# Performance work log

Measured on AMD Instinct MI355X. Metric: run time of the kernel, lower is better.

Reference implementation:

```python
import jax, jax.numpy as jnp
import numpy as np

GROUPS = 8
EPS = 1e-3  # keras GroupNormalization default epsilon


def group_norm(x, gamma, beta):
    # x: [B,H,W,C], groups over channel axis
    B, H, W, C = x.shape
    g = GROUPS
    xr = x.reshape(B, H, W, g, C // g)
    mean = jnp.mean(xr, axis=(1, 2, 4), keepdims=True)
    var = jnp.var(xr, axis=(1, 2, 4), keepdims=True)
    xn = (xr - mean) * jax.lax.rsqrt(var + EPS)
    xn = xn.reshape(B, H, W, C)
    return xn * gamma + beta


def setup_inputs() -> dict:
    key = jax.random.key(0)
    ks = jax.random.split(key, 6)
    B, H, W, C = 8, 64, 64, 64
    std = 0.02
    return {
        "x": jax.random.normal(ks[0], (B, H, W, C), dtype=jnp.float32),
        "gamma": jnp.ones((C,), dtype=jnp.float32),
        "beta": jnp.zeros((C,), dtype=jnp.float32),
        "wq": jax.random.normal(ks[1], (C, C), dtype=jnp.float32) * std,
        "bq": jnp.zeros((C,), dtype=jnp.float32),
        "wk": jax.random.normal(ks[2], (C, C), dtype=jnp.float32) * std,
        "bk": jnp.zeros((C,), dtype=jnp.float32),
        "wv": jax.random.normal(ks[3], (C, C), dtype=jnp.float32) * std,
        "bv": jnp.zeros((C,), dtype=jnp.float32),
        "wp": jax.random.normal(ks[4], (C, C), dtype=jnp.float32) * std,
        "bp": jnp.zeros((C,), dtype=jnp.float32),
    }


def reference(x, gamma, beta, wq, bq, wk, bk, wv, bv, wp, bp):
    B, H, W, C = x.shape
    scale = jnp.asarray(C, x.dtype) ** -0.5
    h = group_norm(x, gamma, beta)  # note: residual uses normalized input (as in source)
    q = h @ wq + bq
    k = h @ wk + bk
    v = h @ wv + bv
    # full O((HW)^2) score tensor, exactly as the original
    attn = jnp.einsum('bhwc,bHWc->bhwHW', q, k) * scale
    attn = jax.nn.softmax(attn.reshape(B, H, W, H * W), axis=-1)
    attn = attn.reshape(B, H, W, H, W)
    proj = jnp.einsum('bhwHW,bHWc->bhwc', attn, v)
    proj = proj @ wp + bp
    return h + proj
```

## Files before the change

kernel.cpp:

```cpp
#include <hip/hip_runtime.h>

#define NTOK 4096
#define CH 64
#define LOG2E 1.4426950408889634f

typedef __bf16 bf8 __attribute__((ext_vector_type(8)));
typedef __bf16 bf4 __attribute__((ext_vector_type(4)));
typedef _Float16 h8 __attribute__((ext_vector_type(8)));
typedef _Float16 h4 __attribute__((ext_vector_type(4)));
typedef __fp16 fp16x2 __attribute__((ext_vector_type(2)));
typedef float f4 __attribute__((ext_vector_type(4)));

__device__ __forceinline__ f4 mfma16(bf8 a, bf8 b, f4 c) {
    return __builtin_amdgcn_mfma_f32_16x16x32_bf16(a, b, c, 0, 0, 0);
}
__device__ __forceinline__ f4 mfma32h(h8 a, h8 b, f4 c) {
    return __builtin_amdgcn_mfma_f32_16x16x32_f16(a, b, c, 0, 0, 0);
}

__global__ __launch_bounds__(256) void pre_kernel(const float* __restrict__ wq,
                                                  const float* __restrict__ wk,
                                                  const float* __restrict__ wv,
                                                  const float* __restrict__ wp,
                                                  const float* __restrict__ x,
                                                  __bf16* __restrict__ wqt,
                                                  __bf16* __restrict__ wkt,
                                                  __bf16* __restrict__ wvt,
                                                  __bf16* __restrict__ wpt,
                                                  float* __restrict__ gpart) {
    int t = threadIdx.x;
    if (blockIdx.x < 4) {
        int m = blockIdx.x;
        const float* src = (m == 0) ? wq : (m == 1) ? wk : (m == 2) ? wv : wp;
        __bf16* dst      = (m == 0) ? wqt : (m == 1) ? wkt : (m == 2) ? wvt : wpt;
        __shared__ float s[64][65];
        for (int i = 0; i < 16; ++i) {
            int e = i * 256 + t;
            s[e >> 6][e & 63] = src[e];
        }
        __syncthreads();
        int o = t >> 2, seg = t & 3;
        for (int j = 0; j < 16; ++j) {
            int in = seg * 16 + j;
            dst[o * 64 + in] = (__bf16)s[in][o];
        }
        return;
    }
    int bid = blockIdx.x - 4;
    int b = bid >> 6, slab = bid & 63;
    const float4* xb = (const float4*)(x + (size_t)(b * NTOK + slab * 64) * CH);
    float s = 0.f, ss = 0.f;
    for (int i = 0; i < 4; ++i) {
        int row = (t >> 4) + i * 16;
        float4 v = xb[row * 16 + (t & 15)];
        s  += v.x + v.y + v.z + v.w;
        ss += v.x * v.x + v.y * v.y + v.z * v.z + v.w * v.w;
    }
    __shared__ float ls[256], lss[256];
    ls[t] = s; lss[t] = ss;
    __syncthreads();
    if (t < 8) {
        float a = 0.f, aa = 0.f;
        for (int p = 0; p < 16; ++p) {
            a  += ls[p * 16 + 2 * t]  + ls[p * 16 + 2 * t + 1];
            aa += lss[p * 16 + 2 * t] + lss[p * 16 + 2 * t + 1];
        }
        gpart[((b * 64 + slab) * 8 + t) * 2 + 0] = a;
        gpart[((b * 64 + slab) * 8 + t) * 2 + 1] = aa;
    }
}

__global__ __launch_bounds__(256) void qkv_gn(const float* __restrict__ x,
                                              const float* __restrict__ gpart,
                                              const float* __restrict__ gamma,
                                              const float* __restrict__ beta,
                                              const __bf16* __restrict__ wqt,
                                              const __bf16* __restrict__ wkt,
                                              const __bf16* __restrict__ wvt,
                                              const float* __restrict__ bq,
                                              const float* __restrict__ bk,
                                              const float* __restrict__ bv,
                                              __bf16* __restrict__ q,
                                              __bf16* __restrict__ k,
                                              _Float16* __restrict__ vT) {
    __shared__ __bf16 W[3][64][72];
    __shared__ __bf16 Hl[64][72];
    __shared__ _Float16 Vst[64][68];
    __shared__ float red[128];
    __shared__ float sstat[16];
    int t = threadIdx.x;
    size_t rowbase = (size_t)blockIdx.x * 64;
    int b = (int)(rowbase >> 12), tokbase = (int)(rowbase & 4095);
    if (t < 64) {
        int gi = t & 7, c = t >> 3;
        const float2* gp = (const float2*)gpart + (size_t)b * 512 + gi;
        float a = 0.f, aa = 0.f;
        for (int p = c * 8; p < c * 8 + 8; ++p) {
            float2 v = gp[(size_t)p * 8];
            a += v.x; aa += v.y;
        }
        red[t * 2] = a; red[t * 2 + 1] = aa;
    }
    for (int m = 0; m < 3; ++m) {
        const __bf16* src = (m == 0) ? wqt : (m == 1) ? wkt : wvt;
        for (int i = 0; i < 2; ++i) {
            int e = i * 256 + t, row = e >> 3, ch = e & 7;
            *(bf8*)&W[m][row][ch * 8] = *(const bf8*)(src + row * 64 + ch * 8);
        }
    }
    __syncthreads();
    if (t < 8) {
        float a = 0.f, aa = 0.f;
        for (int c = 0; c < 8; ++c) {
            a  += red[(c * 8 + t) * 2];
            aa += red[(c * 8 + t) * 2 + 1];
        }
        float mean = a * (1.f / 32768.f);
        float var = aa * (1.f / 32768.f) - mean * mean;
        sstat[t * 2 + 0] = mean;
        sstat[t * 2 + 1] = rsqrtf(var + 1e-3f);
    }
    __syncthreads();
    {
        int c4 = (t & 15) * 4, grp = c4 >> 3;
        float mean = sstat[grp * 2], rstd = sstat[grp * 2 + 1];
        float g0 = gamma[c4] * rstd, g1 = gamma[c4 + 1] * rstd,
              g2 = gamma[c4 + 2] * rstd, g3 = gamma[c4 + 3] * rstd;
        float b0 = beta[c4], b1 = beta[c4 + 1], b2 = beta[c4 + 2], b3 = beta[c4 + 3];
        const float4* xb = (const float4*)(x + rowbase * 64);
        for (int i = 0; i < 4; ++i) {
            int row = (t >> 4) + i * 16;
            float4 v = xb[row * 16 + (t & 15)];
            bf4 hv;
            hv[0] = (__bf16)((v.x - mean) * g0 + b0);
            hv[1] = (__bf16)((v.y - mean) * g1 + b1);
            hv[2] = (__bf16)((v.z - mean) * g2 + b2);
            hv[3] = (__bf16)((v.w - mean) * g3 + b3);
            *(bf4*)&Hl[row][c4] = hv;
        }
    }
    __syncthreads();
    int lane = t & 63, wave = t >> 6, quad = lane >> 4, l15 = lane & 15;
    bf8 a0 = *(const bf8*)&Hl[wave * 16 + l15][quad * 8];
    bf8 a1 = *(const bf8*)&Hl[wave * 16 + l15][32 + quad * 8];
    for (int m = 0; m < 3; ++m) {
        const float* bias = (m == 0) ? bq : (m == 1) ? bk : bv;
        float sc = (m == 0) ? 0.125f * LOG2E : 1.0f;
        for (int tt = 0; tt < 4; ++tt) {
            int col = l15 + 16 * tt;
            bf8 b0 = *(const bf8*)&W[m][col][quad * 8];
            bf8 b1 = *(const bf8*)&W[m][col][32 + quad * 8];
            f4 acc = {0.f, 0.f, 0.f, 0.f};
            acc = mfma16(a0, b0, acc);
            acc = mfma16(a1, b1, acc);
            float bb = bias[col];
            if (m == 2) {
                for (int r = 0; r < 4; ++r)
                    Vst[col][wave * 16 + quad * 4 + r] = (_Float16)(acc[r] + bb);
            } else {
                __bf16* dst = (m == 0) ? q : k;
                for (int r = 0; r < 4; ++r) {
                    float val = (acc[r] + bb) * sc;
                    dst[(rowbase + wave * 16 + quad * 4 + r) * 64 + col] = (__bf16)val;
                }
            }
        }
    }
    __syncthreads();
    {
        int d = wave * 16 + l15;
        for (int kb = 0; kb < 2; ++kb) {
            h4 lo = *(const h4*)&Vst[d][kb * 32 + quad * 4];
            h4 hi = *(const h4*)&Vst[d][kb * 32 + 16 + quad * 4];
            h8 o;
            o[0] = lo[0]; o[1] = lo[1]; o[2] = lo[2]; o[3] = lo[3];
            o[4] = hi[0]; o[5] = hi[1]; o[6] = hi[2]; o[7] = hi[3];
            _Float16* dst = vT + ((((size_t)b * 128 + (tokbase >> 5) + kb) * 4 + wave) * 64
                                  + lane) * 8;
            *(h8*)dst = o;
        }
    }
}

__device__ __forceinline__ void load_kv(const __bf16* kr0, const _Float16* vr, int quad,
                                        bf8 kf[4], h8 vf[4]) {
    kf[0] = *(const bf8*)(kr0 + quad * 8);
    kf[1] = *(const bf8*)(kr0 + 32 + quad * 8);
    kf[2] = *(const bf8*)(kr0 + 1024 + quad * 8);
    kf[3] = *(const bf8*)(kr0 + 1024 + 32 + quad * 8);
    vf[0] = *(const h8*)(vr);
    vf[1] = *(const h8*)(vr + 512);
    vf[2] = *(const h8*)(vr + 1024);
    vf[3] = *(const h8*)(vr + 1536);
}

__device__ __forceinline__ void compute32(const bf8 kf[4], const h8 vf[4],
                                          const bf8 aq[4][2], h8 ones,
                                          f4 acc[4][4], f4 acc_li[4]) {
#pragma unroll
    for (int s = 0; s < 4; ++s) {
        f4 St0 = {0.f, 0.f, 0.f, 0.f};
        f4 St1 = {0.f, 0.f, 0.f, 0.f};
        St0 = mfma16(kf[0], aq[s][0], St0);
        St0 = mfma16(kf[1], aq[s][1], St0);
        St1 = mfma16(kf[2], aq[s][0], St1);
        St1 = mfma16(kf[3], aq[s][1], St1);
        float p00 = __builtin_amdgcn_exp2f(St0[0]);
        float p01 = __builtin_amdgcn_exp2f(St0[1]);
        float p02 = __builtin_amdgcn_exp2f(St0[2]);
        float p03 = __builtin_amdgcn_exp2f(St0[3]);
        float p10 = __builtin_amdgcn_exp2f(St1[0]);
        float p11 = __builtin_amdgcn_exp2f(St1[1]);
        float p12 = __builtin_amdgcn_exp2f(St1[2]);
        float p13 = __builtin_amdgcn_exp2f(St1[3]);
        h8 pf;
        ((fp16x2*)&pf)[0] = __builtin_amdgcn_cvt_pkrtz(p00, p01);
        ((fp16x2*)&pf)[1] = __builtin_amdgcn_cvt_pkrtz(p02, p03);
        ((fp16x2*)&pf)[2] = __builtin_amdgcn_cvt_pkrtz(p10, p11);
        ((fp16x2*)&pf)[3] = __builtin_amdgcn_cvt_pkrtz(p12, p13);
        acc_li[s] = mfma32h(ones, pf, acc_li[s]);
        acc[s][0] = mfma32h(vf[0], pf, acc[s][0]);
        acc[s][1] = mfma32h(vf[1], pf, acc[s][1]);
        acc[s][2] = mfma32h(vf[2], pf, acc[s][2]);
        acc[s][3] = mfma32h(vf[3], pf, acc[s][3]);
    }
}

__global__ __launch_bounds__(256, 2) void attn_final(const __bf16* __restrict__ q,
                                                     const __bf16* __restrict__ k,
                                                     const _Float16* __restrict__ vt,
                                                     const __bf16* __restrict__ wpt,
                                                     const float* __restrict__ bp,
                                                     const float* __restrict__ x,
                                                     const float* __restrict__ gpart,
                                                     const float* __restrict__ gamma,
                                                     const float* __restrict__ beta,
                                                     float* __restrict__ out) {
    __shared__ _Float16 Om[2][64][72];
    __shared__ float sS[2][64];
    __shared__ __bf16 Wl[64][72];
    __shared__ __bf16 Ol[64][72];
    __shared__ float red[128];
    __shared__ float sstat[16], sg[64], sb[64];

    int bid = blockIdx.x;
    int qt = bid >> 3, b = bid & 7;
    int t = threadIdx.x, lane = t & 63, w = t >> 6, quad = lane >> 4, l15 = lane & 15;

    for (int i = 0; i < 2; ++i) {
        int e = i * 256 + t, row = e >> 3, ch = e & 7;
        *(bf8*)&Wl[row][ch * 8] = *(const bf8*)(wpt + row * 64 + ch * 8);
    }
    if (t < 64) { sg[t] = gamma[t]; sb[t] = beta[t]; }
    if (t < 64) {
        int gi = t & 7, c = t >> 3;
        const float2* gp = (const float2*)gpart + (size_t)b * 512 + gi;
        float a = 0.f, aa = 0.f;
        for (int p = c * 8; p < c * 8 + 8; ++p) {
            float2 v = gp[(size_t)p * 8];
            a += v.x; aa += v.y;
        }
        red[t * 2] = a; red[t * 2 + 1] = aa;
    }

    const __bf16* qbase = q + ((size_t)b * NTOK + qt * 64) * 64;
    bf8 aq[4][2];
    for (int s = 0; s < 4; ++s) {
        const __bf16* r = qbase + (s * 16 + l15) * 64;
        aq[s][0] = *(const bf8*)(r + quad * 8);
        aq[s][1] = *(const bf8*)(r + 32 + quad * 8);
    }
    const __bf16* kbase   = k  + ((size_t)b * NTOK + w * 1024) * 64;
    const _Float16* vbase = vt + (size_t)b * 262144 + (size_t)(w * 32) * 2048 + lane * 8;

    h8 ones;
#pragma unroll
    for (int j = 0; j < 8; ++j) ones[j] = (_Float16)1.f;

    f4 acc[4][4] = {};
    f4 acc_li[4] = {};

    bf8 kfA[4], kfB[4];
    h8 vfA[4], vfB[4];
    load_kv(kbase + (size_t)l15 * 64, vbase, quad, kfA, vfA);
    for (int it = 0; it < 32; it += 2) {
        load_kv(kbase + (size_t)((it + 1) * 32 + l15) * 64,
                vbase + (size_t)(it + 1) * 2048, quad, kfB, vfB);
        __builtin_amdgcn_s_setprio(1);
        compute32(kfA, vfA, aq, ones, acc, acc_li);
        __builtin_amdgcn_s_setprio(0);
        if (it + 2 < 32)
            load_kv(kbase + (size_t)((it + 2) * 32 + l15) * 64,
                    vbase + (size_t)(it + 2) * 2048, quad, kfA, vfA);
        __builtin_amdgcn_s_setprio(1);
        compute32(kfB, vfB, aq, ones, acc, acc_li);
        __builtin_amdgcn_s_setprio(0);
    }

    float li[4];
#pragma unroll
    for (int s = 0; s < 4; ++s) li[s] = acc_li[s][0];

    if (w >= 2) {
        for (int s = 0; s < 4; ++s) {
            for (int td = 0; td < 4; ++td) {
                h4 o4;
                for (int r = 0; r < 4; ++r) o4[r] = (_Float16)acc[s][td][r];
                *(h4*)&Om[w - 2][s * 16 + l15][td * 16 + quad * 4] = o4;
            }
            if (quad == 0) sS[w - 2][s * 16 + l15] = li[s];
        }
    }
    __syncthreads();
    if (t < 8) {
        float a = 0.f, aa = 0.f;
        for (int c = 0; c < 8; ++c) {
            a  += red[(c * 8 + t) * 2];
            aa += red[(c * 8 + t) * 2 + 1];
        }
        float mean = a * (1.f / 32768.f);
        float var = aa * (1.f / 32768.f) - mean * mean;
        sstat[t * 2 + 0] = mean;
        sstat[t * 2 + 1] = rsqrtf(var + 1e-3f);
    }
    if (w < 2) {
        for (int s = 0; s < 4; ++s) {
            for (int td = 0; td < 4; ++td) {
                h4 o4 = *(const h4*)&Om[w][s * 16 + l15][td * 16 + quad * 4];
                for (int r = 0; r < 4; ++r) acc[s][td][r] += (float)o4[r];
            }
            li[s] += sS[w][s * 16 + l15];
        }
    }
    __syncthreads();
    if (w < 2) {
        for (int s = 0; s < 4; ++s) {
            for (int td = 0; td < 4; ++td) {
                h4 o4;
                for (int r = 0; r < 4; ++r) o4[r] = (_Float16)acc[s][td][r];
                *(h4*)&Om[w][s * 16 + l15][td * 16 + quad * 4] = o4;
            }
            if (quad == 0) sS[w][s * 16 + l15] = li[s];
        }
    }
    __syncthreads();
    {
        int qq = t >> 2, ds = (t & 3) * 16;
        float inv = 1.f / (sS[0][qq] + sS[1][qq]);
        h8 a0 = *(const h8*)&Om[0][qq][ds];
        h8 b0 = *(const h8*)&Om[0][qq][ds + 8];
        h8 a1 = *(const h8*)&Om[1][qq][ds];
        h8 b1 = *(const h8*)&Om[1][qq][ds + 8];
        bf8 olo, ohi;
        for (int j = 0; j < 8; ++j) {
            olo[j] = (__bf16)(((float)a0[j] + (float)a1[j]) * inv);
            ohi[j] = (__bf16)(((float)b0[j] + (float)b1[j]) * inv);
        }
        *(bf8*)&Ol[qq][ds] = olo;
        *(bf8*)&Ol[qq][ds + 8] = ohi;
    }
    __syncthreads();
    size_t rowbase = ((size_t)b * NTOK + qt * 64) + w * 16;
    bf8 a0 = *(const bf8*)&Ol[w * 16 + l15][quad * 8];
    bf8 a1 = *(const bf8*)&Ol[w * 16 + l15][32 + quad * 8];
    for (int tt = 0; tt < 4; ++tt) {
        int col = l15 + 16 * tt;
        bf8 b0 = *(const bf8*)&Wl[col][quad * 8];
        bf8 b1 = *(const bf8*)&Wl[col][32 + quad * 8];
        f4 pacc = {0.f, 0.f, 0.f, 0.f};
        pacc = mfma16(a0, b0, pacc);
        pacc = mfma16(a1, b1, pacc);
        int grp = col >> 3;
        float mean = sstat[grp * 2], gs = sg[col] * sstat[grp * 2 + 1], bs = sb[col];
        float bias = bp[col];
        for (int r = 0; r < 4; ++r) {
            size_t gi = (rowbase + quad * 4 + r) * 64 + col;
            float h = (x[gi] - mean) * gs + bs;
            out[gi] = pacc[r] + bias + h;
        }
    }
}

extern "C" void kernel_launch(void* const* d_in, const int* in_sizes, int n_in,
                              void* d_out, int out_size, void* d_ws, size_t ws_size,
                              hipStream_t stream) {
    const float* x     = (const float*)d_in[0];
    const float* gamma = (const float*)d_in[1];
    const float* beta  = (const float*)d_in[2];
    const float* wq    = (const float*)d_in[3];
    const float* bq    = (const float*)d_in[4];
    const float* wk    = (const float*)d_in[5];
    const float* bk    = (const float*)d_in[6];
    const float* wv    = (const float*)d_in[7];
    const float* bv    = (const float*)d_in[8];
    const float* wp    = (const float*)d_in[9];
    const float* bp    = (const float*)d_in[10];
    float* out = (float*)d_out;

    char* ws = (char*)d_ws;
    const size_t MB = 1024 * 1024;
    __bf16*   qb   = (__bf16*)(ws);
    __bf16*   kb   = (__bf16*)(ws + 4 * MB);
    _Float16* vtb  = (_Float16*)(ws + 8 * MB);
    __bf16*   wqt  = (__bf16*)(ws + 12 * MB);
    __bf16*   wkt  = (__bf16*)(ws + 12 * MB + 8192);
    __bf16*   wvt  = (__bf16*)(ws + 12 * MB + 16384);
    __bf16*   wpt  = (__bf16*)(ws + 12 * MB + 24576);
    float*    gpart = (float*)(ws + 12 * MB + 32768);

    pre_kernel<<<516, 256, 0, stream>>>(wq, wk, wv, wp, x, wqt, wkt, wvt, wpt, gpart);
    qkv_gn<<<512, 256, 0, stream>>>(x, gpart, gamma, beta, wqt, wkt, wvt, bq, bk, bv, qb, kb, vtb);
    attn_final<<<512, 256, 0, stream>>>(qb, kb, vtb, wpt, bp, x, gpart, gamma, beta, out);
}
```

Before: 134.5 us.

## Split attention key range across eight waves per block instead of four

Doubles the attention block to 512 threads so each of the eight waves processes 512 keys rather than 1024, halving the per-wave serial loop. The partial outputs and row sums are merged in a two-stage shared-memory tree reduction, and the final projection is split across wave halves by column tiles. This raises the waves per CU available to hide latency, at the cost of extra reduction and sync steps and more LDS per block.

```diff
diff --git a/kernel.cpp b/kernel.cpp
--- a/kernel.cpp
+++ b/kernel.cpp
@@ -226,7 +226,7 @@
     }
 }
 
-__global__ __launch_bounds__(256, 2) void attn_final(const __bf16* __restrict__ q,
+__global__ __launch_bounds__(512, 4) void attn_final(const __bf16* __restrict__ q,
                                                      const __bf16* __restrict__ k,
                                                      const _Float16* __restrict__ vt,
                                                      const __bf16* __restrict__ wpt,
@@ -236,8 +236,8 @@
                                                      const float* __restrict__ gamma,
                                                      const float* __restrict__ beta,
                                                      float* __restrict__ out) {
-    __shared__ _Float16 Om[2][64][72];
-    __shared__ float sS[2][64];
+    __shared__ _Float16 Om[4][64][72];
+    __shared__ float sS[4][64];
     __shared__ __bf16 Wl[64][72];
     __shared__ __bf16 Ol[64][72];
     __shared__ float red[128];
@@ -247,11 +247,14 @@
     int qt = bid >> 3, b = bid & 7;
     int t = threadIdx.x, lane = t & 63, w = t >> 6, quad = lane >> 4, l15 = lane & 15;
 
-    for (int i = 0; i < 2; ++i) {
-        int e = i * 256 + t, row = e >> 3, ch = e & 7;
+    if (t < 256) {
+        int e = t * 2;
+        int row = e >> 3, ch = e & 7;
         *(bf8*)&Wl[row][ch * 8] = *(const bf8*)(wpt + row * 64 + ch * 8);
-    }
-    if (t < 64) { sg[t] = gamma[t]; sb[t] = beta[t]; }
+        row = (e + 1) >> 3; ch = (e + 1) & 7;
+        *(bf8*)&Wl[row][ch * 8] = *(const bf8*)(wpt + row * 64 + ch * 8);
+    }
+    if (t >= 256 && t < 320) { int u = t - 256; sg[u] = gamma[u]; sb[u] = beta[u]; }
     if (t < 64) {
         int gi = t & 7, c = t >> 3;
         const float2* gp = (const float2*)gpart + (size_t)b * 512 + gi;
@@ -270,8 +273,8 @@
         aq[s][0] = *(const bf8*)(r + quad * 8);
         aq[s][1] = *(const bf8*)(r + 32 + quad * 8);
     }
-    const __bf16* kbase   = k  + ((size_t)b * NTOK + w * 1024) * 64;
-    const _Float16* vbase = vt + (size_t)b * 262144 + (size_t)(w * 32) * 2048 + lane * 8;
+    const __bf16* kbase   = k  + ((size_t)b * NTOK + w * 512) * 64;
+    const _Float16* vbase = vt + (size_t)b * 262144 + (size_t)(w * 16) * 2048 + lane * 8;
 
     h8 ones;
 #pragma unroll
@@ -283,13 +286,13 @@
     bf8 kfA[4], kfB[4];
     h8 vfA[4], vfB[4];
     load_kv(kbase + (size_t)l15 * 64, vbase, quad, kfA, vfA);
-    for (int it = 0; it < 32; it += 2) {
+    for (int it = 0; it < 16; it += 2) {
         load_kv(kbase + (size_t)((it + 1) * 32 + l15) * 64,
                 vbase + (size_t)(it + 1) * 2048, quad, kfB, vfB);
         __builtin_amdgcn_s_setprio(1);
         compute32(kfA, vfA, aq, ones, acc, acc_li);
         __builtin_amdgcn_s_setprio(0);
-        if (it + 2 < 32)
+        if (it + 2 < 16)
             load_kv(kbase + (size_t)((it + 2) * 32 + l15) * 64,
                     vbase + (size_t)(it + 2) * 2048, quad, kfA, vfA);
         __builtin_amdgcn_s_setprio(1);
@@ -301,7 +304,39 @@
 #pragma unroll
     for (int s = 0; s < 4; ++s) li[s] = acc_li[s][0];
 
-    if (w >= 2) {
+    if (w >= 4) {
+        for (int s = 0; s < 4; ++s) {
+            for (int td = 0; td < 4; ++td) {
+                h4 o4;
+                for (int r = 0; r < 4; ++r) o4[r] = (_Float16)acc[s][td][r];
+                *(h4*)&Om[w - 4][s * 16 + l15][td * 16 + quad * 4] = o4;
+            }
+            if (quad == 0) sS[w - 4][s * 16 + l15] = li[s];
+        }
+    }
+    __syncthreads();
+    if (t < 8) {
+        float a = 0.f, aa = 0.f;
+        for (int c = 0; c < 8; ++c) {
+            a  += red[(c * 8 + t) * 2];
+            aa += red[(c * 8 + t) * 2 + 1];
+        }
+        float mean = a * (1.f / 32768.f);
+        float var = aa * (1.f / 32768.f) - mean * mean;
+        sstat[t * 2 + 0] = mean;
+        sstat[t * 2 + 1] = rsqrtf(var + 1e-3f);
+    }
+    if (w < 4) {
+        for (int s = 0; s < 4; ++s) {
+            for (int td = 0; td < 4; ++td) {
+                h4 o4 = *(const h4*)&Om[w][s * 16 + l15][td * 16 + quad * 4];
+                for (int r = 0; r < 4; ++r) acc[s][td][r] += (float)o4[r];
+            }
+            li[s] += sS[w][s * 16 + l15];
+        }
+    }
+    __syncthreads();
+    if (w >= 2 && w < 4) {
         for (int s = 0; s < 4; ++s) {
             for (int td = 0; td < 4; ++td) {
                 h4 o4;
@@ -312,17 +347,6 @@
         }
     }
     __syncthreads();
-    if (t < 8) {
-        float a = 0.f, aa = 0.f;
-        for (int c = 0; c < 8; ++c) {
-            a  += red[(c * 8 + t) * 2];
-            aa += red[(c * 8 + t) * 2 + 1];
-        }
-        float mean = a * (1.f / 32768.f);
-        float var = aa * (1.f / 32768.f) - mean * mean;
-        sstat[t * 2 + 0] = mean;
-        sstat[t * 2 + 1] = rsqrtf(var + 1e-3f);
-    }
     if (w < 2) {
         for (int s = 0; s < 4; ++s) {
             for (int td = 0; td < 4; ++td) {
@@ -345,38 +369,37 @@
     }
     __syncthreads();
     {
-        int qq = t >> 2, ds = (t & 3) * 16;
+        int qq = t >> 3, ds = (t & 7) * 8;
         float inv = 1.f / (sS[0][qq] + sS[1][qq]);
         h8 a0 = *(const h8*)&Om[0][qq][ds];
-        h8 b0 = *(const h8*)&Om[0][qq][ds + 8];
         h8 a1 = *(const h8*)&Om[1][qq][ds];
-        h8 b1 = *(const h8*)&Om[1][qq][ds + 8];
-        bf8 olo, ohi;
-        for (int j = 0; j < 8; ++j) {
-            olo[j] = (__bf16)(((float)a0[j] + (float)a1[j]) * inv);
-            ohi[j] = (__bf16)(((float)b0[j] + (float)b1[j]) * inv);
-        }
-        *(bf8*)&Ol[qq][ds] = olo;
-        *(bf8*)&Ol[qq][ds + 8] = ohi;
-    }
-    __syncthreads();
-    size_t rowbase = ((size_t)b * NTOK + qt * 64) + w * 16;
-    bf8 a0 = *(const bf8*)&Ol[w * 16 + l15][quad * 8];
-    bf8 a1 = *(const bf8*)&Ol[w * 16 + l15][32 + quad * 8];
-    for (int tt = 0; tt < 4; ++tt) {
-        int col = l15 + 16 * tt;
-        bf8 b0 = *(const bf8*)&Wl[col][quad * 8];
-        bf8 b1 = *(const bf8*)&Wl[col][32 + quad * 8];
-        f4 pacc = {0.f, 0.f, 0.f, 0.f};
-        pacc = mfma16(a0, b0, pacc);
-        pacc = mfma16(a1, b1, pacc);
-        int grp = col >> 3;
-        float mean = sstat[grp * 2], gs = sg[col] * sstat[grp * 2 + 1], bs = sb[col];
-        float bias = bp[col];
-        for (int r = 0; r < 4; ++r) {
-            size_t gi = (rowbase + quad * 4 + r) * 64 + col;
-            float h = (x[gi] - mean) * gs + bs;
-            out[gi] = pacc[r] + bias + h;
+        bf8 o;
+        for (int j = 0; j < 8; ++j)
+            o[j] = (__bf16)(((float)a0[j] + (float)a1[j]) * inv);
+        *(bf8*)&Ol[qq][ds] = o;
+    }
+    __syncthreads();
+    {
+        int wr = w & 3, wh = w >> 2;
+        size_t rowbase = ((size_t)b * NTOK + qt * 64) + wr * 16;
+        bf8 a0 = *(const bf8*)&Ol[wr * 16 + l15][quad * 8];
+        bf8 a1 = *(const bf8*)&Ol[wr * 16 + l15][32 + quad * 8];
+        for (int tth = 0; tth < 2; ++tth) {
+            int tt = wh * 2 + tth;
+            int col = l15 + 16 * tt;
+            bf8 b0 = *(const bf8*)&Wl[col][quad * 8];
+            bf8 b1 = *(const bf8*)&Wl[col][32 + quad * 8];
+            f4 pacc = {0.f, 0.f, 0.f, 0.f};
+            pacc = mfma16(a0, b0, pacc);
+            pacc = mfma16(a1, b1, pacc);
+            int grp = col >> 3;
+            float mean = sstat[grp * 2], gs = sg[col] * sstat[grp * 2 + 1], bs = sb[col];
+            float bias = bp[col];
+            for (int r = 0; r < 4; ++r) {
+                size_t gi = (rowbase + quad * 4 + r) * 64 + col;
+                float h = (x[gi] - mean) * gs + bs;
+                out[gi] = pacc[r] + bias + h;
+            }
         }
     }
 }
@@ -410,5 +433,5 @@
 
     pre_kernel<<<516, 256, 0, stream>>>(wq, wk, wv, wp, x, wqt, wkt, wvt, wpt, gpart);
     qkv_gn<<<512, 256, 0, stream>>>(x, gpart, gamma, beta, wqt, wkt, wvt, bq, bk, bv, qb, kb, vtb);
-    attn_final<<<512, 256, 0, stream>>>(qb, kb, vtb, wpt, bp, x, gpart, gamma, beta, out);
-}
+    attn_final<<<512, 512, 0, stream>>>(qb, kb, vtb, wpt, bp, x, gpart, gamma, beta, out);
+}
```

New measurement: 523.7 us. 289% more time.

## Switch attention QK and PV matmuls to FP8 MFMA with prepacked K/V

Applied to the files above, without the earlier changes.

Q, K, V and the softmax probabilities are quantized to FP8 (e4m3) and both attention matmuls use the 16x16x32 fp8 MFMA instead of bf16/f16. The scale sqrt(scale*log2e) is applied to both Q and K, and K/V are written in a lane-packed layout so each load is one 16-byte vector. This halves the bytes of K/V traffic and register footprint and uses the higher-rate FP8 matrix path. In exchange it adds conversion instructions and loses precision in the scores, probabilities and V, which risks exceeding the accuracy tolerance.

```diff
diff --git a/kernel.cpp b/kernel.cpp
--- a/kernel.cpp
+++ b/kernel.cpp
@@ -3,19 +3,23 @@
 #define NTOK 4096
 #define CH 64
 #define LOG2E 1.4426950408889634f
+#define QK_SCALE 0.42466090014400953f
 
 typedef __bf16 bf8 __attribute__((ext_vector_type(8)));
 typedef __bf16 bf4 __attribute__((ext_vector_type(4)));
 typedef _Float16 h8 __attribute__((ext_vector_type(8)));
 typedef _Float16 h4 __attribute__((ext_vector_type(4)));
-typedef __fp16 fp16x2 __attribute__((ext_vector_type(2)));
 typedef float f4 __attribute__((ext_vector_type(4)));
+typedef long lx2 __attribute__((ext_vector_type(2)));
 
 __device__ __forceinline__ f4 mfma16(bf8 a, bf8 b, f4 c) {
     return __builtin_amdgcn_mfma_f32_16x16x32_bf16(a, b, c, 0, 0, 0);
 }
-__device__ __forceinline__ f4 mfma32h(h8 a, h8 b, f4 c) {
-    return __builtin_amdgcn_mfma_f32_16x16x32_f16(a, b, c, 0, 0, 0);
+__device__ __forceinline__ f4 mfma8(long a, long b, f4 c) {
+    return __builtin_amdgcn_mfma_f32_16x16x32_fp8_fp8(a, b, c, 0, 0, 0);
+}
+__device__ __forceinline__ unsigned char to_fp8(float v) {
+    return (unsigned char)(__builtin_amdgcn_cvt_pk_fp8_f32(v, v, 0, false) & 0xff);
 }
 
 __global__ __launch_bounds__(256) void pre_kernel(const float* __restrict__ wq,
@@ -80,12 +84,13 @@
                                               const float* __restrict__ bq,
                                               const float* __restrict__ bk,
                                               const float* __restrict__ bv,
-                                              __bf16* __restrict__ q,
-                                              __bf16* __restrict__ k,
-                                              _Float16* __restrict__ vT) {
+                                              unsigned char* __restrict__ qf,
+                                              unsigned char* __restrict__ kp,
+                                              unsigned char* __restrict__ vp) {
     __shared__ __bf16 W[3][64][72];
     __shared__ __bf16 Hl[64][72];
     __shared__ _Float16 Vst[64][68];
+    __shared__ unsigned char Kst[64][72];
     __shared__ float red[128];
     __shared__ float sstat[16];
     int t = threadIdx.x;
@@ -145,7 +150,7 @@
     bf8 a1 = *(const bf8*)&Hl[wave * 16 + l15][32 + quad * 8];
     for (int m = 0; m < 3; ++m) {
         const float* bias = (m == 0) ? bq : (m == 1) ? bk : bv;
-        float sc = (m == 0) ? 0.125f * LOG2E : 1.0f;
+        float sc = (m == 2) ? 1.0f : QK_SCALE;
         for (int tt = 0; tt < 4; ++tt) {
             int col = l15 + 16 * tt;
             bf8 b0 = *(const bf8*)&W[m][col][quad * 8];
@@ -157,54 +162,63 @@
             if (m == 2) {
                 for (int r = 0; r < 4; ++r)
                     Vst[col][wave * 16 + quad * 4 + r] = (_Float16)(acc[r] + bb);
+            } else if (m == 1) {
+                for (int r = 0; r < 4; ++r)
+                    Kst[wave * 16 + quad * 4 + r][col] = to_fp8((acc[r] + bb) * sc);
             } else {
-                __bf16* dst = (m == 0) ? q : k;
                 for (int r = 0; r < 4; ++r) {
                     float val = (acc[r] + bb) * sc;
-                    dst[(rowbase + wave * 16 + quad * 4 + r) * 64 + col] = (__bf16)val;
+                    qf[(rowbase + wave * 16 + quad * 4 + r) * 64 + col] = to_fp8(val);
                 }
             }
         }
     }
     __syncthreads();
+    {
+        const unsigned char* row = &Kst[wave * 16 + l15][0];
+        long lo = *(const long*)(row + quad * 8);
+        long hi = *(const long*)(row + 32 + quad * 8);
+        lx2 kk; kk[0] = lo; kk[1] = hi;
+        *(lx2*)(kp + (((size_t)b * 256 + (tokbase >> 4) + wave) * 64 + lane) * 16) = kk;
+    }
     {
         int d = wave * 16 + l15;
         for (int kb = 0; kb < 2; ++kb) {
             h4 lo = *(const h4*)&Vst[d][kb * 32 + quad * 4];
             h4 hi = *(const h4*)&Vst[d][kb * 32 + 16 + quad * 4];
-            h8 o;
-            o[0] = lo[0]; o[1] = lo[1]; o[2] = lo[2]; o[3] = lo[3];
-            o[4] = hi[0]; o[5] = hi[1]; o[6] = hi[2]; o[7] = hi[3];
-            _Float16* dst = vT + ((((size_t)b * 128 + (tokbase >> 5) + kb) * 4 + wave) * 64
-                                  + lane) * 8;
-            *(h8*)dst = o;
-        }
-    }
-}
-
-__device__ __forceinline__ void load_kv(const __bf16* kr0, const _Float16* vr, int quad,
-                                        bf8 kf[4], h8 vf[4]) {
-    kf[0] = *(const bf8*)(kr0 + quad * 8);
-    kf[1] = *(const bf8*)(kr0 + 32 + quad * 8);
-    kf[2] = *(const bf8*)(kr0 + 1024 + quad * 8);
-    kf[3] = *(const bf8*)(kr0 + 1024 + 32 + quad * 8);
-    vf[0] = *(const h8*)(vr);
-    vf[1] = *(const h8*)(vr + 512);
-    vf[2] = *(const h8*)(vr + 1024);
-    vf[3] = *(const h8*)(vr + 1536);
-}
-
-__device__ __forceinline__ void compute32(const bf8 kf[4], const h8 vf[4],
-                                          const bf8 aq[4][2], h8 ones,
-                                          f4 acc[4][4], f4 acc_li[4]) {
+            int d0 = __builtin_amdgcn_cvt_pk_fp8_f32((float)lo[0], (float)lo[1], 0, false);
+            d0     = __builtin_amdgcn_cvt_pk_fp8_f32((float)lo[2], (float)lo[3], d0, true);
+            int d1 = __builtin_amdgcn_cvt_pk_fp8_f32((float)hi[0], (float)hi[1], 0, false);
+            d1     = __builtin_amdgcn_cvt_pk_fp8_f32((float)hi[2], (float)hi[3], d1, true);
+            long v8 = (long)(unsigned int)d0 | ((long)d1 << 32);
+            int kt = (tokbase >> 5) + kb;
+            *(long*)(vp + ((((size_t)b * 128 + kt) * 2 + (wave >> 1)) * 64 + lane) * 16
+                        + (wave & 1) * 8) = v8;
+        }
+    }
+}
+
+__device__ __forceinline__ void load_kv(const unsigned char* kpw, const unsigned char* vpw,
+                                        long kf[4], long vf[4]) {
+    lx2 a = *(const lx2*)(kpw);
+    lx2 b = *(const lx2*)(kpw + 1024);
+    lx2 c = *(const lx2*)(vpw);
+    lx2 d = *(const lx2*)(vpw + 1024);
+    kf[0] = a[0]; kf[1] = a[1]; kf[2] = b[0]; kf[3] = b[1];
+    vf[0] = c[0]; vf[1] = c[1]; vf[2] = d[0]; vf[3] = d[1];
+}
+
+__device__ __forceinline__ void compute32(const long kf[4], const long vf[4],
+                                          const long aqlo[4], const long aqhi[4],
+                                          long ones, f4 acc[4][4], f4 acc_li[4]) {
 #pragma unroll
     for (int s = 0; s < 4; ++s) {
         f4 St0 = {0.f, 0.f, 0.f, 0.f};
         f4 St1 = {0.f, 0.f, 0.f, 0.f};
-        St0 = mfma16(kf[0], aq[s][0], St0);
-        St0 = mfma16(kf[1], aq[s][1], St0);
-        St1 = mfma16(kf[2], aq[s][0], St1);
-        St1 = mfma16(kf[3], aq[s][1], St1);
+        St0 = mfma8(kf[0], aqlo[s], St0);
+        St0 = mfma8(kf[1], aqhi[s], St0);
+        St1 = mfma8(kf[2], aqlo[s], St1);
+        St1 = mfma8(kf[3], aqhi[s], St1);
         float p00 = __builtin_amdgcn_exp2f(St0[0]);
         float p01 = __builtin_amdgcn_exp2f(St0[1]);
         float p02 = __builtin_amdgcn_exp2f(St0[2]);
@@ -213,22 +227,22 @@
         float p11 = __builtin_amdgcn_exp2f(St1[1]);
         float p12 = __builtin_amdgcn_exp2f(St1[2]);
         float p13 = __builtin_amdgcn_exp2f(St1[3]);
-        h8 pf;
-        ((fp16x2*)&pf)[0] = __builtin_amdgcn_cvt_pkrtz(p00, p01);
-        ((fp16x2*)&pf)[1] = __builtin_amdgcn_cvt_pkrtz(p02, p03);
-        ((fp16x2*)&pf)[2] = __builtin_amdgcn_cvt_pkrtz(p10, p11);
-        ((fp16x2*)&pf)[3] = __builtin_amdgcn_cvt_pkrtz(p12, p13);
-        acc_li[s] = mfma32h(ones, pf, acc_li[s]);
-        acc[s][0] = mfma32h(vf[0], pf, acc[s][0]);
-        acc[s][1] = mfma32h(vf[1], pf, acc[s][1]);
-        acc[s][2] = mfma32h(vf[2], pf, acc[s][2]);
-        acc[s][3] = mfma32h(vf[3], pf, acc[s][3]);
-    }
-}
-
-__global__ __launch_bounds__(256, 2) void attn_final(const __bf16* __restrict__ q,
-                                                     const __bf16* __restrict__ k,
-                                                     const _Float16* __restrict__ vt,
+        int d0 = __builtin_amdgcn_cvt_pk_fp8_f32(p00, p01, 0, false);
+        d0     = __builtin_amdgcn_cvt_pk_fp8_f32(p02, p03, d0, true);
+        int d1 = __builtin_amdgcn_cvt_pk_fp8_f32(p10, p11, 0, false);
+        d1     = __builtin_amdgcn_cvt_pk_fp8_f32(p12, p13, d1, true);
+        long pf = (long)(unsigned int)d0 | ((long)d1 << 32);
+        acc_li[s] = mfma8(ones, pf, acc_li[s]);
+        acc[s][0] = mfma8(vf[0], pf, acc[s][0]);
+        acc[s][1] = mfma8(vf[1], pf, acc[s][1]);
+        acc[s][2] = mfma8(vf[2], pf, acc[s][2]);
+        acc[s][3] = mfma8(vf[3], pf, acc[s][3]);
+    }
+}
+
+__global__ __launch_bounds__(256, 2) void attn_final(const unsigned char* __restrict__ qf,
+                                                     const unsigned char* __restrict__ kp,
+                                                     const unsigned char* __restrict__ vp,
                                                      const __bf16* __restrict__ wpt,
                                                      const float* __restrict__ bp,
                                                      const float* __restrict__ x,
@@ -263,37 +277,32 @@
         red[t * 2] = a; red[t * 2 + 1] = aa;
     }
 
-    const __bf16* qbase = q + ((size_t)b * NTOK + qt * 64) * 64;
-    bf8 aq[4][2];
+    const unsigned char* qbase = qf + ((size_t)b * NTOK + qt * 64) * 64;
+    long aqlo[4], aqhi[4];
     for (int s = 0; s < 4; ++s) {
-        const __bf16* r = qbase + (s * 16 + l15) * 64;
-        aq[s][0] = *(const bf8*)(r + quad * 8);
-        aq[s][1] = *(const bf8*)(r + 32 + quad * 8);
-    }
-    const __bf16* kbase   = k  + ((size_t)b * NTOK + w * 1024) * 64;
-    const _Float16* vbase = vt + (size_t)b * 262144 + (size_t)(w * 32) * 2048 + lane * 8;
-
-    h8 ones;
-#pragma unroll
-    for (int j = 0; j < 8; ++j) ones[j] = (_Float16)1.f;
+        const unsigned char* r = qbase + (size_t)(s * 16 + l15) * 64;
+        aqlo[s] = *(const long*)(r + quad * 8);
+        aqhi[s] = *(const long*)(r + 32 + quad * 8);
+    }
+    const unsigned char* kpw = kp + ((size_t)b * 256 + w * 64) * 1024 + lane * 16;
+    const unsigned char* vpw = vp + ((size_t)b * 128 + w * 32) * 2048 + lane * 16;
+
+    const long ones = 0x3838383838383838L;
 
     f4 acc[4][4] = {};
     f4 acc_li[4] = {};
 
-    bf8 kfA[4], kfB[4];
-    h8 vfA[4], vfB[4];
-    load_kv(kbase + (size_t)l15 * 64, vbase, quad, kfA, vfA);
+    long kfA[4], kfB[4], vfA[4], vfB[4];
+    load_kv(kpw, vpw, kfA, vfA);
     for (int it = 0; it < 32; it += 2) {
-        load_kv(kbase + (size_t)((it + 1) * 32 + l15) * 64,
-                vbase + (size_t)(it + 1) * 2048, quad, kfB, vfB);
+        load_kv(kpw + (size_t)(it + 1) * 2048, vpw + (size_t)(it + 1) * 2048, kfB, vfB);
         __builtin_amdgcn_s_setprio(1);
-        compute32(kfA, vfA, aq, ones, acc, acc_li);
+        compute32(kfA, vfA, aqlo, aqhi, ones, acc, acc_li);
         __builtin_amdgcn_s_setprio(0);
         if (it + 2 < 32)
-            load_kv(kbase + (size_t)((it + 2) * 32 + l15) * 64,
-                    vbase + (size_t)(it + 2) * 2048, quad, kfA, vfA);
+            load_kv(kpw + (size_t)(it + 2) * 2048, vpw + (size_t)(it + 2) * 2048, kfA, vfA);
         __builtin_amdgcn_s_setprio(1);
-        compute32(kfB, vfB, aq, ones, acc, acc_li);
+        compute32(kfB, vfB, aqlo, aqhi, ones, acc, acc_li);
         __builtin_amdgcn_s_setprio(0);
     }
 
@@ -399,9 +408,9 @@
 
     char* ws = (char*)d_ws;
     const size_t MB = 1024 * 1024;
-    __bf16*   qb   = (__bf16*)(ws);
-    __bf16*   kb   = (__bf16*)(ws + 4 * MB);
-    _Float16* vtb  = (_Float16*)(ws + 8 * MB);
+    unsigned char* qfb = (unsigned char*)(ws);
+    unsigned char* kpb = (unsigned char*)(ws + 2 * MB);
+    unsigned char* vpb = (unsigned char*)(ws + 4 * MB);
     __bf16*   wqt  = (__bf16*)(ws + 12 * MB);
     __bf16*   wkt  = (__bf16*)(ws + 12 * MB + 8192);
     __bf16*   wvt  = (__bf16*)(ws + 12 * MB + 16384);
@@ -409,6 +418,7 @@
     float*    gpart = (float*)(ws + 12 * MB + 32768);
 
     pre_kernel<<<516, 256, 0, stream>>>(wq, wk, wv, wp, x, wqt, wkt, wvt, wpt, gpart);
-    qkv_gn<<<512, 256, 0, stream>>>(x, gpart, gamma, beta, wqt, wkt, wvt, bq, bk, bv, qb, kb, vtb);
-    attn_final<<<512, 256, 0, stream>>>(qb, kb, vtb, wpt, bp, x, gpart, gamma, beta, out);
-}
+    qkv_gn<<<512, 256, 0, stream>>>(x, gpart, gamma, beta, wqt, wkt, wvt, bq, bk, bv,
+                                    qfb, kpb, vpb);
+    attn_final<<<512, 256, 0, stream>>>(qfb, kpb, vpb, wpt, bp, x, gpart, gamma, beta, out);
+}
```

New measurement: 120.7 us. 1.11x faster.
